# Performance work log

Measured on AMD Instinct MI355X. Metric: run time of the kernel, lower is better.

The kernel has to match this reference:

```python
import jax, jax.numpy as jnp
import numpy as np

GRID_RES = 128      # dense voxel grid standing in for octree leaves
BASIS_DIM = 9       # SH degree 2
DATA_DIM = 3 * BASIS_DIM + 1  # 27 SH color coeffs + 1 density
N_RAYS = 65536
N_STEPS = 128       # fixed ray-marching steps (replaces per-voxel traversal)
STEP_SIZE = 0.001
BG = 1.0            # background_brightness


def sh_basis9(d):
    # real SH basis, deg <= 2, svox component order/signs. d: [B,3] unit dirs
    x, y, z = d[..., 0], d[..., 1], d[..., 2]
    xx, yy, zz = x * x, y * y, z * z
    return jnp.stack([
        jnp.full_like(x, 0.28209479177387814),
        -0.4886025119029199 * y,
        0.4886025119029199 * z,
        -0.4886025119029199 * x,
        1.0925484305920792 * x * y,
        -1.0925484305920792 * y * z,
        0.31539156525252005 * (2.0 * zz - xx - yy),
        -1.0925484305920792 * x * z,
        0.5462742152960396 * (xx - yy),
    ], axis=-1)


def dda_unit(cen, invdir):
    # ray/unit-cube AABB intersection, vectorized over rays
    t1 = -cen * invdir
    t2 = t1 + invdir
    tmin = jnp.maximum(jnp.max(jnp.minimum(t1, t2), axis=-1), 0.0)
    tmax = jnp.minimum(jnp.min(jnp.maximum(t1, t2), axis=-1), 1e9)
    return tmin, tmax


def setup_inputs() -> dict:
    key = jax.random.key(0)
    k1, k2, k3, k4 = jax.random.split(key, 4)
    data = jax.random.normal(k1, (GRID_RES, GRID_RES, GRID_RES, DATA_DIM), jnp.float32) * 0.5
    origins = jax.random.uniform(k2, (N_RAYS, 3), jnp.float32, 0.1, 0.9)
    dirs = jax.random.normal(k3, (N_RAYS, 3), jnp.float32)
    viewdirs = jax.random.normal(k4, (N_RAYS, 3), jnp.float32)
    return {"data": data, "origins": origins, "dirs": dirs, "viewdirs": viewdirs}


def reference(data, origins, dirs, viewdirs):
    dirs = dirs / jnp.linalg.norm(dirs, axis=-1, keepdims=True)
    viewdirs = viewdirs / jnp.linalg.norm(viewdirs, axis=-1, keepdims=True)
    invdirs = 1.0 / (dirs + 1e-9)
    tmin, tmax = dda_unit(origins, invdirs)        # [B], [B]
    dt = jnp.maximum(tmax - tmin, 0.0) / N_STEPS   # per-ray step length
    delta_t = dt + STEP_SIZE                       # eps per step, as in svox
    sh_mult = sh_basis9(viewdirs)                  # [B, BASIS_DIM]
    B = origins.shape[0]

    def step(carry, i):
        light, out = carry                         # [B], [B,3]
        t = tmin + (i.astype(jnp.float32) + 0.5) * dt
        pos = origins + t[:, None] * dirs          # [B,3] in [0,1]
        idx = jnp.clip((pos * GRID_RES).astype(jnp.int32), 0, GRID_RES - 1)
        vals = data[idx[:, 0], idx[:, 1], idx[:, 2]]  # [B, DATA_DIM]
        sigma = jax.nn.relu(vals[:, -1])
        att = jnp.exp(-delta_t * sigma)
        weight = light * (1.0 - att)
        rgb_sh = vals[:, :-1].reshape(B, 3, BASIS_DIM)
        rgb = jax.nn.sigmoid(jnp.einsum('bk,bck->bc', sh_mult, rgb_sh))
        out = out + weight[:, None] * rgb
        return (light * att, out), None

    init = (jnp.ones((B,), jnp.float32), jnp.zeros((B, 3), jnp.float32))
    (light, out), _ = jax.lax.scan(step, init, jnp.arange(N_STEPS))
    return out + BG * light[:, None]
```

## Files before the change

### kernel.cpp

```cpp
#include <hip/hip_runtime.h>

#define GRID_RES 128
#define N_RAYS 65536
#define N_STEPS 128
#define STEP_SIZE 0.001f

__device__ __forceinline__ float sigmoidf_fast(float x) {
    return 1.0f / (1.0f + __expf(-x));
}

__device__ __forceinline__ float quad_dpp_xor1(float x) {
    return __int_as_float(__builtin_amdgcn_update_dpp(0, __float_as_int(x), 0xB1, 0xF, 0xF, true));
}
__device__ __forceinline__ float quad_dpp_xor2(float x) {
    return __int_as_float(__builtin_amdgcn_update_dpp(0, __float_as_int(x), 0x4E, 0xF, 0xF, true));
}
__device__ __forceinline__ float quad_bcast3(float x) {
    return __int_as_float(__builtin_amdgcn_update_dpp(0, __float_as_int(x), 0xFF, 0xF, 0xF, true));
}
__device__ __forceinline__ float quad_sum(float x) {
    x += quad_dpp_xor1(x);
    x += quad_dpp_xor2(x);
    return x;
}

__global__ __launch_bounds__(256) void vr_kernel(
    const float* __restrict__ data,
    const float* __restrict__ origins,
    const float* __restrict__ dirs,
    const float* __restrict__ viewdirs,
    float* __restrict__ out)
{
    int gid = blockIdx.x * blockDim.x + threadIdx.x;
    int ray = gid >> 2;
    int l   = gid & 3;

    float ox = origins[3*ray+0], oy = origins[3*ray+1], oz = origins[3*ray+2];
    float dx = dirs[3*ray+0],    dy = dirs[3*ray+1],    dz = dirs[3*ray+2];
    float vx = viewdirs[3*ray+0], vy = viewdirs[3*ray+1], vz = viewdirs[3*ray+2];

    {
        float s = __fadd_rn(__fadd_rn(__fmul_rn(dx,dx), __fmul_rn(dy,dy)), __fmul_rn(dz,dz));
        float n = sqrtf(s);
        dx = __fdiv_rn(dx, n); dy = __fdiv_rn(dy, n); dz = __fdiv_rn(dz, n);
    }
    {
        float s = __fadd_rn(__fadd_rn(__fmul_rn(vx,vx), __fmul_rn(vy,vy)), __fmul_rn(vz,vz));
        float n = sqrtf(s);
        vx = __fdiv_rn(vx, n); vy = __fdiv_rn(vy, n); vz = __fdiv_rn(vz, n);
    }

    float invx = __fdiv_rn(1.0f, __fadd_rn(dx, 1e-9f));
    float invy = __fdiv_rn(1.0f, __fadd_rn(dy, 1e-9f));
    float invz = __fdiv_rn(1.0f, __fadd_rn(dz, 1e-9f));

    float t1x = __fmul_rn(-ox, invx), t1y = __fmul_rn(-oy, invy), t1z = __fmul_rn(-oz, invz);
    float t2x = __fadd_rn(t1x, invx), t2y = __fadd_rn(t1y, invy), t2z = __fadd_rn(t1z, invz);
    float tmin = fmaxf(fmaxf(fminf(t1x,t2x), fminf(t1y,t2y)), fminf(t1z,t2z));
    tmin = fmaxf(tmin, 0.0f);
    float tmax = fminf(fminf(fmaxf(t1x,t2x), fmaxf(t1y,t2y)), fmaxf(t1z,t2z));
    tmax = fminf(tmax, 1e9f);
    float dt = __fmul_rn(fmaxf(__fsub_rn(tmax, tmin), 0.0f), (1.0f/(float)N_STEPS));
    float delta_t = __fadd_rn(dt, STEP_SIZE);

    const float sh0 = 0.28209479177387814f;
    float sh1 = -0.4886025119029199f * vy;
    float sh2 =  0.4886025119029199f * vz;
    float sh3 = -0.4886025119029199f * vx;
    float sh4 =  1.0925484305920792f * vx * vy;
    float sh5 = -1.0925484305920792f * vy * vz;
    float sh6 =  0.31539156525252005f * (2.0f*vz*vz - vx*vx - vy*vy);
    float sh7 = -1.0925484305920792f * vx * vz;
    float sh8 =  0.5462742152960396f * (vx*vx - vy*vy);

    float wr[8], wg[8], wb[8];
    #pragma unroll
    for (int m = 0; m < 8; ++m) {
        int c  = 8*l + m;
        int cb = c % 9;
        float s = sh0;
        s = (cb==1) ? sh1 : s;
        s = (cb==2) ? sh2 : s;
        s = (cb==3) ? sh3 : s;
        s = (cb==4) ? sh4 : s;
        s = (cb==5) ? sh5 : s;
        s = (cb==6) ? sh6 : s;
        s = (cb==7) ? sh7 : s;
        s = (cb==8) ? sh8 : s;
        wr[m] = (c < 9)            ? s : 0.0f;
        wg[m] = (c >= 9 && c < 18) ? s : 0.0f;
        wb[m] = (c >= 18 && c < 27)? s : 0.0f;
    }

    unsigned offA = 8u * (unsigned)l;
    unsigned offB = (l < 3) ? (8u * (unsigned)l + 4u) : 24u;

    float light = 1.0f;
    float o_r = 0.0f, o_g = 0.0f, o_b = 0.0f;

    #pragma unroll 2
    for (int i = 0; i < N_STEPS; ++i) {
        float t = __fadd_rn(tmin, __fmul_rn((float)i + 0.5f, dt));
        float px = __fadd_rn(ox, __fmul_rn(t, dx));
        float py = __fadd_rn(oy, __fmul_rn(t, dy));
        float pz = __fadd_rn(oz, __fmul_rn(t, dz));
        int ix = (int)(px * (float)GRID_RES);
        int iy = (int)(py * (float)GRID_RES);
        int iz = (int)(pz * (float)GRID_RES);
        ix = min(max(ix, 0), GRID_RES-1);
        iy = min(max(iy, 0), GRID_RES-1);
        iz = min(max(iz, 0), GRID_RES-1);
        unsigned lin = (unsigned)(((ix << 7) | iy) << 7 | iz);

        const float* rec = data + 28u * lin;
        float4 A = *(const float4*)(rec + offA);
        float4 B = *(const float4*)(rec + offB);

        float pr = wr[0]*A.x + wr[1]*A.y + wr[2]*A.z + wr[3]*A.w
                 + wr[4]*B.x + wr[5]*B.y + wr[6]*B.z + wr[7]*B.w;
        float pg = wg[0]*A.x + wg[1]*A.y + wg[2]*A.z + wg[3]*A.w
                 + wg[4]*B.x + wg[5]*B.y + wg[6]*B.z + wg[7]*B.w;
        float pb = wb[0]*A.x + wb[1]*A.y + wb[2]*A.z + wb[3]*A.w
                 + wb[4]*B.x + wb[5]*B.y + wb[6]*B.z + wb[7]*B.w;

        float r = quad_sum(pr);
        float g = quad_sum(pg);
        float b = quad_sum(pb);
        float sigma = fmaxf(quad_bcast3(A.w), 0.0f);

        float att = __expf(-delta_t * sigma);
        float w = light * (1.0f - att);

        o_r = fmaf(w, sigmoidf_fast(r), o_r);
        o_g = fmaf(w, sigmoidf_fast(g), o_g);
        o_b = fmaf(w, sigmoidf_fast(b), o_b);
        light *= att;
    }

    if (l == 0) {
        out[3*ray+0] = o_r + light;
        out[3*ray+1] = o_g + light;
        out[3*ray+2] = o_b + light;
    }
}

extern "C" void kernel_launch(void* const* d_in, const int* in_sizes, int n_in,
                              void* d_out, int out_size, void* d_ws, size_t ws_size,
                              hipStream_t stream) {
    const float* data     = (const float*)d_in[0];
    const float* origins  = (const float*)d_in[1];
    const float* dirs     = (const float*)d_in[2];
    const float* viewdirs = (const float*)d_in[3];
    float* out = (float*)d_out;

    dim3 block(256);
    dim3 grid((N_RAYS * 4) / 256);
    vr_kernel<<<grid, block, 0, stream>>>(data, origins, dirs, viewdirs, out);
}
```

Baseline: 138.1 us.

## Software-pipeline voxel gathers and redirect zero-density steps to a shared record

The ray-march loop now prefetches the density of the voxel two steps ahead and the full SH record one step ahead, so gather latency overlaps the current step's math. Each lane loads density directly instead of getting it through a DPP broadcast. When density is non-positive, the record load is pointed at the start of the data buffer so that cache line stays hot, saving bandwidth on empty voxels whose weight is zero anyway. This adds a dependent density load ahead of each record load, more live registers, and one extra gather per lane per step.

```diff
diff --git a/kernel.cpp b/kernel.cpp
--- a/kernel.cpp
+++ b/kernel.cpp
@@ -14,9 +14,6 @@
 }
 __device__ __forceinline__ float quad_dpp_xor2(float x) {
     return __int_as_float(__builtin_amdgcn_update_dpp(0, __float_as_int(x), 0x4E, 0xF, 0xF, true));
-}
-__device__ __forceinline__ float quad_bcast3(float x) {
-    return __int_as_float(__builtin_amdgcn_update_dpp(0, __float_as_int(x), 0xFF, 0xF, 0xF, true));
 }
 __device__ __forceinline__ float quad_sum(float x) {
     x += quad_dpp_xor1(x);
@@ -95,11 +92,7 @@
     unsigned offA = 8u * (unsigned)l;
     unsigned offB = (l < 3) ? (8u * (unsigned)l + 4u) : 24u;
 
-    float light = 1.0f;
-    float o_r = 0.0f, o_g = 0.0f, o_b = 0.0f;
-
-    #pragma unroll 2
-    for (int i = 0; i < N_STEPS; ++i) {
+    auto linidx = [&](int i) -> unsigned {
         float t = __fadd_rn(tmin, __fmul_rn((float)i + 0.5f, dt));
         float px = __fadd_rn(ox, __fmul_rn(t, dx));
         float py = __fadd_rn(oy, __fmul_rn(t, dy));
@@ -110,31 +103,56 @@
         ix = min(max(ix, 0), GRID_RES-1);
         iy = min(max(iy, 0), GRID_RES-1);
         iz = min(max(iz, 0), GRID_RES-1);
-        unsigned lin = (unsigned)(((ix << 7) | iy) << 7 | iz);
+        return (unsigned)(((ix << 7) | iy) << 7 | iz);
+    };
 
-        const float* rec = data + 28u * lin;
-        float4 A = *(const float4*)(rec + offA);
-        float4 B = *(const float4*)(rec + offB);
+    float light = 1.0f;
+    float o_r = 0.0f, o_g = 0.0f, o_b = 0.0f;
 
-        float pr = wr[0]*A.x + wr[1]*A.y + wr[2]*A.z + wr[3]*A.w
-                 + wr[4]*B.x + wr[5]*B.y + wr[6]*B.z + wr[7]*B.w;
-        float pg = wg[0]*A.x + wg[1]*A.y + wg[2]*A.z + wg[3]*A.w
-                 + wg[4]*B.x + wg[5]*B.y + wg[6]*B.z + wg[7]*B.w;
-        float pb = wb[0]*A.x + wb[1]*A.y + wb[2]*A.z + wb[3]*A.w
-                 + wb[4]*B.x + wb[5]*B.y + wb[6]*B.z + wb[7]*B.w;
+    unsigned lin1;
+    float s0, s1;
+    float4 A0, B0;
+    {
+        unsigned lin0 = linidx(0);
+        lin1 = linidx(1);
+        s0 = data[28u * lin0 + 27u];
+        s1 = data[28u * lin1 + 27u];
+        const float* rec0 = (s0 > 0.0f) ? (data + 28u * lin0) : data;
+        A0 = *(const float4*)(rec0 + offA);
+        B0 = *(const float4*)(rec0 + offB);
+    }
+
+    for (int i = 0; i < N_STEPS; ++i) {
+        unsigned lin2 = linidx(i + 2);
+        float s2 = data[28u * lin2 + 27u];
+
+        const float* rec1 = (s1 > 0.0f) ? (data + 28u * lin1) : data;
+        float4 A1 = *(const float4*)(rec1 + offA);
+        float4 B1 = *(const float4*)(rec1 + offB);
+
+        float sigma = fmaxf(s0, 0.0f);
+        float att = __expf(-delta_t * sigma);
+        float w = light * (1.0f - att);
+
+        float pr = wr[0]*A0.x + wr[1]*A0.y + wr[2]*A0.z + wr[3]*A0.w
+                 + wr[4]*B0.x + wr[5]*B0.y + wr[6]*B0.z + wr[7]*B0.w;
+        float pg = wg[0]*A0.x + wg[1]*A0.y + wg[2]*A0.z + wg[3]*A0.w
+                 + wg[4]*B0.x + wg[5]*B0.y + wg[6]*B0.z + wg[7]*B0.w;
+        float pb = wb[0]*A0.x + wb[1]*A0.y + wb[2]*A0.z + wb[3]*A0.w
+                 + wb[4]*B0.x + wb[5]*B0.y + wb[6]*B0.z + wb[7]*B0.w;
 
         float r = quad_sum(pr);
         float g = quad_sum(pg);
         float b = quad_sum(pb);
-        float sigma = fmaxf(quad_bcast3(A.w), 0.0f);
-
-        float att = __expf(-delta_t * sigma);
-        float w = light * (1.0f - att);
 
         o_r = fmaf(w, sigmoidf_fast(r), o_r);
         o_g = fmaf(w, sigmoidf_fast(g), o_g);
         o_b = fmaf(w, sigmoidf_fast(b), o_b);
         light *= att;
+
+        s0 = s1; s1 = s2;
+        lin1 = lin2;
+        A0 = A1; B0 = B1;
     }
 
     if (l == 0) {
```

New measurement: 122.0 us. 1.13x faster.

## Software-pipeline voxel loads and skip color fetch for non-positive density

Applied to the files above, without the earlier changes.

Restructures the march loop into a software pipeline. The density word is loaded four steps ahead and the color float4 pairs two steps ahead, so memory latency overlaps with shading of earlier steps. Color loads for samples whose density is not positive are redirected to the start of the data buffer, which stays cache-resident; their weight is zero anyway, so random-gather traffic drops. It also uses a hardware reciprocal in the sigmoid and adds an occupancy hint to launch_bounds. The cost is more live registers for the in-flight loads and a small accuracy change from the approximate reciprocal.

```diff
diff --git a/kernel.cpp b/kernel.cpp
--- a/kernel.cpp
+++ b/kernel.cpp
@@ -5,8 +5,11 @@
 #define N_STEPS 128
 #define STEP_SIZE 0.001f
 
+__device__ __forceinline__ float rcp_fast(float x) {
+    return __builtin_amdgcn_rcpf(x);
+}
 __device__ __forceinline__ float sigmoidf_fast(float x) {
-    return 1.0f / (1.0f + __expf(-x));
+    return rcp_fast(1.0f + __expf(-x));
 }
 
 __device__ __forceinline__ float quad_dpp_xor1(float x) {
@@ -15,16 +18,13 @@
 __device__ __forceinline__ float quad_dpp_xor2(float x) {
     return __int_as_float(__builtin_amdgcn_update_dpp(0, __float_as_int(x), 0x4E, 0xF, 0xF, true));
 }
-__device__ __forceinline__ float quad_bcast3(float x) {
-    return __int_as_float(__builtin_amdgcn_update_dpp(0, __float_as_int(x), 0xFF, 0xF, 0xF, true));
-}
 __device__ __forceinline__ float quad_sum(float x) {
     x += quad_dpp_xor1(x);
     x += quad_dpp_xor2(x);
     return x;
 }
 
-__global__ __launch_bounds__(256) void vr_kernel(
+__global__ __launch_bounds__(256, 4) void vr_kernel(
     const float* __restrict__ data,
     const float* __restrict__ origins,
     const float* __restrict__ dirs,
@@ -73,7 +73,7 @@
     float sh7 = -1.0925484305920792f * vx * vz;
     float sh8 =  0.5462742152960396f * (vx*vx - vy*vy);
 
-    float wr[8], wg[8], wb[8];
+    float wr[8], wg_[8], wb[8];
     #pragma unroll
     for (int m = 0; m < 8; ++m) {
         int c  = 8*l + m;
@@ -87,19 +87,15 @@
         s = (cb==6) ? sh6 : s;
         s = (cb==7) ? sh7 : s;
         s = (cb==8) ? sh8 : s;
-        wr[m] = (c < 9)            ? s : 0.0f;
-        wg[m] = (c >= 9 && c < 18) ? s : 0.0f;
-        wb[m] = (c >= 18 && c < 27)? s : 0.0f;
+        wr[m]  = (c < 9)            ? s : 0.0f;
+        wg_[m] = (c >= 9 && c < 18) ? s : 0.0f;
+        wb[m]  = (c >= 18 && c < 27)? s : 0.0f;
     }
 
     unsigned offA = 8u * (unsigned)l;
     unsigned offB = (l < 3) ? (8u * (unsigned)l + 4u) : 24u;
 
-    float light = 1.0f;
-    float o_r = 0.0f, o_g = 0.0f, o_b = 0.0f;
-
-    #pragma unroll 2
-    for (int i = 0; i < N_STEPS; ++i) {
+    auto linidx = [&](int i) -> unsigned {
         float t = __fadd_rn(tmin, __fmul_rn((float)i + 0.5f, dt));
         float px = __fadd_rn(ox, __fmul_rn(t, dx));
         float py = __fadd_rn(oy, __fmul_rn(t, dy));
@@ -110,31 +106,72 @@
         ix = min(max(ix, 0), GRID_RES-1);
         iy = min(max(iy, 0), GRID_RES-1);
         iz = min(max(iz, 0), GRID_RES-1);
-        unsigned lin = (unsigned)(((ix << 7) | iy) << 7 | iz);
+        return (unsigned)(((ix << 7) | iy) << 7 | iz);
+    };
 
-        const float* rec = data + 28u * lin;
-        float4 A = *(const float4*)(rec + offA);
-        float4 B = *(const float4*)(rec + offB);
+    float light = 1.0f;
+    float o_r = 0.0f, o_g = 0.0f, o_b = 0.0f;
+
+    auto shade = [&](float s, const float4& A, const float4& B) {
+        float sigma = fmaxf(s, 0.0f);
+        float att = __expf(-delta_t * sigma);
+        float w = light * (1.0f - att);
 
         float pr = wr[0]*A.x + wr[1]*A.y + wr[2]*A.z + wr[3]*A.w
                  + wr[4]*B.x + wr[5]*B.y + wr[6]*B.z + wr[7]*B.w;
-        float pg = wg[0]*A.x + wg[1]*A.y + wg[2]*A.z + wg[3]*A.w
-                 + wg[4]*B.x + wg[5]*B.y + wg[6]*B.z + wg[7]*B.w;
+        float pg = wg_[0]*A.x + wg_[1]*A.y + wg_[2]*A.z + wg_[3]*A.w
+                 + wg_[4]*B.x + wg_[5]*B.y + wg_[6]*B.z + wg_[7]*B.w;
         float pb = wb[0]*A.x + wb[1]*A.y + wb[2]*A.z + wb[3]*A.w
                  + wb[4]*B.x + wb[5]*B.y + wb[6]*B.z + wb[7]*B.w;
 
         float r = quad_sum(pr);
         float g = quad_sum(pg);
         float b = quad_sum(pb);
-        float sigma = fmaxf(quad_bcast3(A.w), 0.0f);
-
-        float att = __expf(-delta_t * sigma);
-        float w = light * (1.0f - att);
 
         o_r = fmaf(w, sigmoidf_fast(r), o_r);
         o_g = fmaf(w, sigmoidf_fast(g), o_g);
         o_b = fmaf(w, sigmoidf_fast(b), o_b);
         light *= att;
+    };
+
+    float sA, sB, sC, sD;
+    float4 CAa, CAb, CBa, CBb;
+    unsigned linP, linQ;
+    {
+        unsigned lin0 = linidx(0), lin1 = linidx(1);
+        linP = linidx(2); linQ = linidx(3);
+        sA = data[28u*lin0 + 27u];
+        sB = data[28u*lin1 + 27u];
+        sC = data[28u*linP + 27u];
+        sD = data[28u*linQ + 27u];
+        const float* r0 = (sA > 0.0f) ? (data + 28u*lin0) : data;
+        CAa = *(const float4*)(r0 + offA);
+        CAb = *(const float4*)(r0 + offB);
+        const float* r1 = (sB > 0.0f) ? (data + 28u*lin1) : data;
+        CBa = *(const float4*)(r1 + offA);
+        CBb = *(const float4*)(r1 + offB);
+    }
+
+    #pragma unroll 1
+    for (int i = 0; i < N_STEPS; i += 2) {
+        unsigned lin4 = linidx(i + 4);
+        unsigned lin5 = linidx(i + 5);
+        float sE = data[28u*lin4 + 27u];
+        float sF = data[28u*lin5 + 27u];
+
+        const float* rp = (sC > 0.0f) ? (data + 28u*linP) : data;
+        float4 CCa = *(const float4*)(rp + offA);
+        float4 CCb = *(const float4*)(rp + offB);
+        const float* rq = (sD > 0.0f) ? (data + 28u*linQ) : data;
+        float4 CDa = *(const float4*)(rq + offA);
+        float4 CDb = *(const float4*)(rq + offB);
+
+        shade(sA, CAa, CAb);
+        shade(sB, CBa, CBb);
+
+        sA = sC; sB = sD; sC = sE; sD = sF;
+        CAa = CCa; CAb = CCb; CBa = CDa; CBb = CDb;
+        linP = lin4; linQ = lin5;
     }
 
     if (l == 0) {
```

Result: faster. 129.4 us (-6.3%).

## Repack voxel grid into 64-byte fp16 records before ray marching

Applied to the files above, without the earlier changes.

Adds a pre-pass kernel that converts each 28-float voxel record into a 64-byte fp16 record with ReLU already applied to density, stored in workspace. The march kernel then does one aligned 16-byte load per lane per step instead of two float4 loads from a 112-byte stride. It also switches sigmoid to a hardware reciprocal, raises unroll to 4 and adds an occupancy hint. The repack reads the full grid and writes a new one on every call, which may cost more than the smaller gathers save, and fp16 storage lowers accuracy.

```diff
diff --git a/kernel.cpp b/kernel.cpp
--- a/kernel.cpp
+++ b/kernel.cpp
@@ -1,12 +1,17 @@
 #include <hip/hip_runtime.h>
+#include <hip/hip_fp16.h>
 
 #define GRID_RES 128
 #define N_RAYS 65536
 #define N_STEPS 128
 #define STEP_SIZE 0.001f
-
+#define NVOX (GRID_RES * GRID_RES * GRID_RES)
+
+__device__ __forceinline__ float rcp_fast(float x) {
+    return __builtin_amdgcn_rcpf(x);
+}
 __device__ __forceinline__ float sigmoidf_fast(float x) {
-    return 1.0f / (1.0f + __expf(-x));
+    return rcp_fast(1.0f + __expf(-x));
 }
 
 __device__ __forceinline__ float quad_dpp_xor1(float x) {
@@ -24,8 +29,36 @@
     return x;
 }
 
-__global__ __launch_bounds__(256) void vr_kernel(
-    const float* __restrict__ data,
+__device__ __forceinline__ unsigned pack2(float a, float b) {
+    return ((unsigned)__half_as_ushort(__float2half(b)) << 16)
+         |  (unsigned)__half_as_ushort(__float2half(a));
+}
+
+__global__ __launch_bounds__(256) void repack_kernel(
+    const float* __restrict__ data, uint4* __restrict__ packed)
+{
+    unsigned v = blockIdx.x * 256u + threadIdx.x;
+    const float4* rec = (const float4*)(data + 28u * v);
+    float4 c0 = rec[0], c1 = rec[1], c2 = rec[2], c3 = rec[3],
+           c4 = rec[4], c5 = rec[5], c6 = rec[6];
+    float sig = fmaxf(c6.w, 0.0f);
+
+    uint4 q0, q1, q2, q3;
+    q0.x = pack2(c0.x, c0.y); q0.y = pack2(c0.z, c0.w);
+    q0.z = pack2(c1.x, c1.y); q0.w = pack2(c1.z, c1.w);
+    q1.x = pack2(c2.x, c2.y); q1.y = pack2(c2.z, c2.w);
+    q1.z = pack2(c3.x, c3.y); q1.w = pack2(c3.z, c3.w);
+    q2.x = pack2(c4.x, c4.y); q2.y = pack2(c4.z, c4.w);
+    q2.z = pack2(c5.x, c5.y); q2.w = pack2(c5.z, c5.w);
+    q3.x = pack2(c6.x, c6.y); q3.y = pack2(c6.z, sig);
+    q3.z = 0u; q3.w = 0u;
+
+    uint4* dst = packed + 4u * v;
+    dst[0] = q0; dst[1] = q1; dst[2] = q2; dst[3] = q3;
+}
+
+__global__ __launch_bounds__(256, 4) void vr_kernel(
+    const uint4* __restrict__ packed,
     const float* __restrict__ origins,
     const float* __restrict__ dirs,
     const float* __restrict__ viewdirs,
@@ -73,7 +106,7 @@
     float sh7 = -1.0925484305920792f * vx * vz;
     float sh8 =  0.5462742152960396f * (vx*vx - vy*vy);
 
-    float wr[8], wg[8], wb[8];
+    float wr[8], wg_[8], wb[8];
     #pragma unroll
     for (int m = 0; m < 8; ++m) {
         int c  = 8*l + m;
@@ -87,19 +120,12 @@
         s = (cb==6) ? sh6 : s;
         s = (cb==7) ? sh7 : s;
         s = (cb==8) ? sh8 : s;
-        wr[m] = (c < 9)            ? s : 0.0f;
-        wg[m] = (c >= 9 && c < 18) ? s : 0.0f;
-        wb[m] = (c >= 18 && c < 27)? s : 0.0f;
-    }
-
-    unsigned offA = 8u * (unsigned)l;
-    unsigned offB = (l < 3) ? (8u * (unsigned)l + 4u) : 24u;
-
-    float light = 1.0f;
-    float o_r = 0.0f, o_g = 0.0f, o_b = 0.0f;
-
-    #pragma unroll 2
-    for (int i = 0; i < N_STEPS; ++i) {
+        wr[m]  = (c < 9)            ? s : 0.0f;
+        wg_[m] = (c >= 9 && c < 18) ? s : 0.0f;
+        wb[m]  = (c >= 18 && c < 27)? s : 0.0f;
+    }
+
+    auto linidx = [&](int i) -> unsigned {
         float t = __fadd_rn(tmin, __fmul_rn((float)i + 0.5f, dt));
         float px = __fadd_rn(ox, __fmul_rn(t, dx));
         float py = __fadd_rn(oy, __fmul_rn(t, dy));
@@ -110,26 +136,40 @@
         ix = min(max(ix, 0), GRID_RES-1);
         iy = min(max(iy, 0), GRID_RES-1);
         iz = min(max(iz, 0), GRID_RES-1);
-        unsigned lin = (unsigned)(((ix << 7) | iy) << 7 | iz);
-
-        const float* rec = data + 28u * lin;
-        float4 A = *(const float4*)(rec + offA);
-        float4 B = *(const float4*)(rec + offB);
-
-        float pr = wr[0]*A.x + wr[1]*A.y + wr[2]*A.z + wr[3]*A.w
-                 + wr[4]*B.x + wr[5]*B.y + wr[6]*B.z + wr[7]*B.w;
-        float pg = wg[0]*A.x + wg[1]*A.y + wg[2]*A.z + wg[3]*A.w
-                 + wg[4]*B.x + wg[5]*B.y + wg[6]*B.z + wg[7]*B.w;
-        float pb = wb[0]*A.x + wb[1]*A.y + wb[2]*A.z + wb[3]*A.w
-                 + wb[4]*B.x + wb[5]*B.y + wb[6]*B.z + wb[7]*B.w;
+        return (unsigned)(((ix << 7) | iy) << 7 | iz);
+    };
+
+    float light = 1.0f;
+    float o_r = 0.0f, o_g = 0.0f, o_b = 0.0f;
+
+    #pragma unroll 4
+    for (int i = 0; i < N_STEPS; ++i) {
+        unsigned lin = linidx(i);
+        uint4 q = packed[4u * lin + (unsigned)l];
+
+        float f0 = __half2float(__ushort_as_half((unsigned short)(q.x)));
+        float f1 = __half2float(__ushort_as_half((unsigned short)(q.x >> 16)));
+        float f2 = __half2float(__ushort_as_half((unsigned short)(q.y)));
+        float f3 = __half2float(__ushort_as_half((unsigned short)(q.y >> 16)));
+        float f4 = __half2float(__ushort_as_half((unsigned short)(q.z)));
+        float f5 = __half2float(__ushort_as_half((unsigned short)(q.z >> 16)));
+        float f6 = __half2float(__ushort_as_half((unsigned short)(q.w)));
+        float f7 = __half2float(__ushort_as_half((unsigned short)(q.w >> 16)));
+
+        float sigma = quad_bcast3(f3);
+        float att = __expf(-delta_t * sigma);
+        float w = light * (1.0f - att);
+
+        float pr = wr[0]*f0 + wr[1]*f1 + wr[2]*f2 + wr[3]*f3
+                 + wr[4]*f4 + wr[5]*f5 + wr[6]*f6 + wr[7]*f7;
+        float pg = wg_[0]*f0 + wg_[1]*f1 + wg_[2]*f2 + wg_[3]*f3
+                 + wg_[4]*f4 + wg_[5]*f5 + wg_[6]*f6 + wg_[7]*f7;
+        float pb = wb[0]*f0 + wb[1]*f1 + wb[2]*f2 + wb[3]*f3
+                 + wb[4]*f4 + wb[5]*f5 + wb[6]*f6 + wb[7]*f7;
 
         float r = quad_sum(pr);
         float g = quad_sum(pg);
         float b = quad_sum(pb);
-        float sigma = fmaxf(quad_bcast3(A.w), 0.0f);
-
-        float att = __expf(-delta_t * sigma);
-        float w = light * (1.0f - att);
 
         o_r = fmaf(w, sigmoidf_fast(r), o_r);
         o_g = fmaf(w, sigmoidf_fast(g), o_g);
@@ -153,7 +193,8 @@
     const float* viewdirs = (const float*)d_in[3];
     float* out = (float*)d_out;
 
-    dim3 block(256);
-    dim3 grid((N_RAYS * 4) / 256);
-    vr_kernel<<<grid, block, 0, stream>>>(data, origins, dirs, viewdirs, out);
-}
+    uint4* packed = (uint4*)d_ws;
+
+    repack_kernel<<<NVOX / 256, 256, 0, stream>>>(data, packed);
+    vr_kernel<<<(N_RAYS * 4) / 256, 256, 0, stream>>>(packed, origins, dirs, viewdirs, out);
+}
```

Result: slower. 155.4 us (+12.6%).
